# Optimization experiments

Measured on AMD Instinct MI355X. Metric: run time of the kernel, lower is better.

## Reference

```python
import jax, jax.numpy as jnp
import numpy as np

WS = 8          # window size
NUM_HEADS = 12


def setup_inputs() -> dict:
    key = jax.random.key(0)
    k1, k2, k3 = jax.random.split(key, 3)
    B, N, C = 16, 4096, 384
    x = jax.random.normal(k1, (B, N, C), dtype=jnp.float32)
    # torch Linear weights stored as [in, out] so forward is x @ W
    qkv_w = jax.random.normal(k2, (C, 3 * C), dtype=jnp.float32) * (C ** -0.5)
    proj_w = jax.random.normal(k3, (C, C), dtype=jnp.float32) * (C ** -0.5)
    proj_b = jnp.zeros((C,), dtype=jnp.float32)
    return {"x": x, "qkv_w": qkv_w, "proj_w": proj_w, "proj_b": proj_b}


def reference(x, qkv_w, proj_w, proj_b):
    B, N, C = x.shape
    H = W = int(np.sqrt(N))
    hg, wg = H // WS, W // WS
    G = hg * wg
    nh = NUM_HEADS
    hd = C // nh
    scale = hd ** -0.5

    # window partition: [B, N, C] -> [B, hg, wg, ws, ws, C]
    xw = x.reshape(B, hg, WS, wg, WS, C).transpose(0, 1, 3, 2, 4, 5)
    xw = xw.reshape(B, G, WS * WS, C)

    # qkv projection -> [3, B, G, nh, ws*ws, hd]
    qkv = (xw @ qkv_w).reshape(B, G, WS * WS, 3, nh, hd)
    qkv = qkv.transpose(3, 0, 1, 4, 2, 5)
    q, k, v = qkv[0], qkv[1], qkv[2]

    attn = jnp.einsum('bgnqd,bgnkd->bgnqk', q, k) * scale
    attn = jax.nn.softmax(attn, axis=-1)
    out = jnp.einsum('bgnqk,bgnkd->bgnqd', attn, v)

    # merge heads and reverse window partition
    out = out.transpose(0, 1, 3, 2, 4).reshape(B, hg, wg, WS, WS, C)
    out = out.transpose(0, 1, 3, 2, 4, 5).reshape(B, N, C)

    return out @ proj_w + proj_b
```

## Files before the change

kernel.cpp:

```cpp
#include <hip/hip_runtime.h>
#include <stdint.h>

typedef unsigned short ushort_t;
typedef __bf16 bf16x8 __attribute__((ext_vector_type(8)));
typedef float floatx4 __attribute__((ext_vector_type(4)));
typedef unsigned short ushort8 __attribute__((ext_vector_type(8)));

__device__ __forceinline__ ushort_t f2b(float f) {
  union { float f; unsigned u; } v; v.f = f;
  unsigned r = v.u + 0x7fffu + ((v.u >> 16) & 1u);
  return (ushort_t)(r >> 16);
}
__device__ __forceinline__ ushort_t b2u(float f) {
  union { __bf16 b; ushort_t u; } v; v.b = (__bf16)f; return v.u;
}
__device__ __forceinline__ bf16x8 cvt8(const float* p) {
  floatx4 f0 = *(const floatx4*)p;
  floatx4 f1 = *(const floatx4*)(p + 4);
  union { bf16x8 v; __bf16 e[8]; } u;
#pragma unroll
  for (int j = 0; j < 4; ++j) u.e[j] = (__bf16)f0[j];
#pragma unroll
  for (int j = 0; j < 4; ++j) u.e[4 + j] = (__bf16)f1[j];
  return u.v;
}

__device__ __forceinline__ void async16(const ushort_t* g, ushort_t* l) {
  __builtin_amdgcn_global_load_lds(
      (const __attribute__((address_space(1))) void*)g,
      (__attribute__((address_space(3))) void*)l, 16, 0, 0);
}

__global__ __launch_bounds__(256) void cvt_x(const float* __restrict__ src,
                                             ushort_t* __restrict__ dst, int n8) {
  int i = blockIdx.x * 256 + threadIdx.x;
  if (i < n8) *(bf16x8*)&dst[(size_t)i * 8] = cvt8(src + (size_t)i * 8);
}

__global__ void transpose_k(const float* __restrict__ src,
                            ushort_t* __restrict__ dst, int R, int Cc) {
  int idx = blockIdx.x * 256 + threadIdx.x;
  if (idx < R * Cc) {
    int r = idx / Cc, c = idx % Cc;
    dst[(size_t)c * R + r] = f2b(src[idx]);
  }
}

template <int C_F32>
__global__ __launch_bounds__(256) void gemm_bt(
    const ushort_t* __restrict__ A, int lda,
    const ushort_t* __restrict__ Bt,
    const float* __restrict__ bias, void* __restrict__ C_,
    int M, int N, int K) {
  __shared__ __align__(16) ushort_t As[128 * 64];
  __shared__ __align__(16) ushort_t Bs[128 * 64];
  const int t = threadIdx.x;

  const int nwg = gridDim.x;
  const int per = nwg >> 3;
  const int swz = (blockIdx.x & 7) * per + (blockIdx.x >> 3);
  const int ntn = N >> 7;
  const int m0 = (swz / ntn) << 7;
  const int n0 = (swz % ntn) << 7;

  const int w = t >> 6, lane = t & 63;
  const int wy = (w >> 1) << 6;
  const int wx = (w & 1) << 6;
  const int l15 = lane & 15;
  const int quad = lane >> 4;
  const int quad4 = quad << 2;

  floatx4 acc[4][4] = {};

  const int srow = t >> 3;
  const int sc = (((t & 7) ^ (srow & 7)) << 3);
  const ushort_t* gA = A + (size_t)(m0 + srow) * lda + sc;
  const ushort_t* gB = Bt + (size_t)(n0 + srow) * K + sc;

  for (int k0 = 0; k0 < K; k0 += 64) {
    __syncthreads();
#pragma unroll
    for (int r4 = 0; r4 < 4; ++r4) {
      async16(gA + (size_t)r4 * 32 * lda + k0, &As[r4 * 2048 + t * 8]);
      async16(gB + (size_t)r4 * 32 * K + k0, &Bs[r4 * 2048 + t * 8]);
    }
    __syncthreads();
#pragma unroll
    for (int kk = 0; kk < 2; ++kk) {
      bf16x8 af[4], bfr[4];
#pragma unroll
      for (int i = 0; i < 4; ++i) {
        int row = wy + i * 16 + l15;
        af[i] = *(const bf16x8*)&As[row * 64 + ((((kk << 2) | quad) ^ (row & 7)) << 3)];
      }
#pragma unroll
      for (int j = 0; j < 4; ++j) {
        int row = wx + j * 16 + l15;
        bfr[j] = *(const bf16x8*)&Bs[row * 64 + ((((kk << 2) | quad) ^ (row & 7)) << 3)];
      }
#pragma unroll
      for (int i = 0; i < 4; ++i)
#pragma unroll
        for (int j = 0; j < 4; ++j)
          acc[i][j] = __builtin_amdgcn_mfma_f32_16x16x32_bf16(
              af[i], bfr[j], acc[i][j], 0, 0, 0);
    }
  }

  float bv[4] = {0.f, 0.f, 0.f, 0.f};
  if (bias != nullptr) {
#pragma unroll
    for (int j = 0; j < 4; ++j) bv[j] = bias[n0 + wx + j * 16 + l15];
  }
#pragma unroll
  for (int i = 0; i < 4; ++i) {
#pragma unroll
    for (int r = 0; r < 4; ++r) {
      size_t row = (size_t)(m0 + wy + i * 16 + quad4 + r);
      if (C_F32) {
        float* cp = (float*)C_ + row * N + (n0 + wx + l15);
#pragma unroll
        for (int j = 0; j < 4; ++j) cp[j * 16] = acc[i][j][r] + bv[j];
      } else {
        ushort_t* cp = (ushort_t*)C_ + row * N + (n0 + wx + l15);
#pragma unroll
        for (int j = 0; j < 4; ++j) cp[j * 16] = f2b(acc[i][j][r] + bv[j]);
      }
    }
  }
}

__global__ __launch_bounds__(256, 2) void win_attn(
    const ushort_t* __restrict__ QKV, ushort_t* __restrict__ O, int ostride) {
  __shared__ __align__(16) ushort_t Plds[4][64 * 40];
  __shared__ __align__(16) ushort_t Vt[4][32 * 72];
  const int blk = blockIdx.x;
  const int b = blk >> 6, g = blk & 63;
  const int gy = g >> 3, gx = g & 7;
  const int t = threadIdx.x, w = t >> 6, lane = t & 63;
  const int l15 = lane & 15, quad = lane >> 4;
  const int q8 = quad << 3, quad4 = quad << 2;
  const size_t bbase = (size_t)b * 4096 + (size_t)(gy * 8) * 64 + gx * 8;
  const float scale = 0.17677669529663687f;

  bf16x8 ones;
  {
    union { bf16x8 v; __bf16 e[8]; } u;
#pragma unroll
    for (int j = 0; j < 8; ++j) u.e[j] = (__bf16)1.0f;
    ones = u.v;
  }

  for (int hi = 0; hi < 3; ++hi) {
    const int h = w * 3 + hi;
    const size_t hq = (size_t)h * 32;

    {
      size_t row = bbase + (size_t)(lane >> 3) * 64 + (lane & 7);
      const ushort_t* vp = QKV + row * 1152 + 768 + hq;
#pragma unroll
      for (int i = 0; i < 4; ++i) {
        ushort8 vv = *(const ushort8*)(vp + i * 8);
#pragma unroll
        for (int j = 0; j < 8; ++j) Vt[w][(i * 8 + j) * 72 + lane] = vv[j];
      }
    }

    bf16x8 qf[4], kf[4];
#pragma unroll
    for (int i = 0; i < 4; ++i) {
      int tok = i * 16 + l15;
      size_t row = bbase + (size_t)(tok >> 3) * 64 + (tok & 7);
      qf[i] = *(const bf16x8*)(QKV + row * 1152 + hq + q8);
      kf[i] = *(const bf16x8*)(QKV + row * 1152 + 384 + hq + q8);
    }

    floatx4 s[4][4] = {};
#pragma unroll
    for (int i = 0; i < 4; ++i)
#pragma unroll
      for (int j = 0; j < 4; ++j)
        s[i][j] = __builtin_amdgcn_mfma_f32_16x16x32_bf16(
            qf[i], kf[j], s[i][j], 0, 0, 0);

    floatx4 o[4][2] = {};
    floatx4 osum[4] = {};
#pragma unroll
    for (int ks = 0; ks < 2; ++ks) {
#pragma unroll
      for (int i = 0; i < 4; ++i) {
#pragma unroll
        for (int r = 0; r < 4; ++r) {
          float p0 = __expf(s[i][2 * ks][r] * scale);
          float p1 = __expf(s[i][2 * ks + 1][r] * scale);
          int pr = (i * 16 + quad4 + r) * 40 + l15;
          Plds[w][pr] = b2u(p0);
          Plds[w][pr + 16] = b2u(p1);
        }
      }
      bf16x8 pf[4], vf[2];
#pragma unroll
      for (int i = 0; i < 4; ++i)
        pf[i] = *(const bf16x8*)&Plds[w][(i * 16 + l15) * 40 + q8];
#pragma unroll
      for (int j = 0; j < 2; ++j)
        vf[j] = *(const bf16x8*)&Vt[w][(j * 16 + l15) * 72 + ks * 32 + q8];
#pragma unroll
      for (int i = 0; i < 4; ++i) {
#pragma unroll
        for (int j = 0; j < 2; ++j)
          o[i][j] = __builtin_amdgcn_mfma_f32_16x16x32_bf16(
              pf[i], vf[j], o[i][j], 0, 0, 0);
        osum[i] = __builtin_amdgcn_mfma_f32_16x16x32_bf16(
            pf[i], ones, osum[i], 0, 0, 0);
      }
    }

#pragma unroll
    for (int i = 0; i < 4; ++i) {
#pragma unroll
      for (int r = 0; r < 4; ++r) {
        int tok = i * 16 + quad4 + r;
        size_t row = bbase + (size_t)(tok >> 3) * 64 + (tok & 7);
        float inv = 1.0f / osum[i][r];
        ushort_t* op = O + row * (size_t)ostride + hq;
#pragma unroll
        for (int j = 0; j < 2; ++j) op[j * 16 + l15] = b2u(o[i][j][r] * inv);
      }
    }
  }
}

extern "C" void kernel_launch(void* const* d_in, const int* in_sizes, int n_in,
                              void* d_out, int out_size, void* d_ws, size_t ws_size,
                              hipStream_t stream) {
  const float* x      = (const float*)d_in[0];
  const float* qkv_w  = (const float*)d_in[1];
  const float* proj_w = (const float*)d_in[2];
  const float* proj_b = (const float*)d_in[3];
  float* out = (float*)d_out;

  const int M = 16 * 4096;
  const size_t need =
      ((size_t)M * 1152 + (size_t)M * 384 + 1152 * 384 + 384 * 384) * 2;
  if (ws_size < need) return;

  ushort_t* qkv    = (ushort_t*)d_ws;
  ushort_t* xb     = qkv + (size_t)M * 1152;
  ushort_t* qkvwT  = xb + (size_t)M * 384;
  ushort_t* projwT = qkvwT + (size_t)1152 * 384;

  cvt_x<<<(M * 384 / 8 + 255) / 256, 256, 0, stream>>>(x, xb, M * 384 / 8);
  transpose_k<<<(384 * 1152 + 255) / 256, 256, 0, stream>>>(qkv_w, qkvwT, 384, 1152);
  transpose_k<<<(384 * 384 + 255) / 256, 256, 0, stream>>>(proj_w, projwT, 384, 384);

  gemm_bt<0><<<(M / 128) * (1152 / 128), 256, 0, stream>>>(
      xb, 384, qkvwT, nullptr, qkv, M, 1152, 384);

  win_attn<<<16 * 64, 256, 0, stream>>>(qkv, qkv, 1152);

  gemm_bt<1><<<(M / 128) * (384 / 128), 256, 0, stream>>>(
      qkv, 1152, projwT, proj_b, out, M, 384, 384);
}
```

Measured before the change: 337.3 us.

## Add 8-wave triple-buffered pipelined GEMM with interleaved prefetch for both projections

Adds a new GEMM kernel with 512 threads and 256x128 tiles. It triple-buffers LDS through dynamic shared memory, so async global-to-LDS loads for tile k+2 are issued while MFMAs run on tile k. The block splits compute into four phases that interleave prefetch issue, barriers and s_setprio around MFMA groups, replacing the old load-then-compute loop with two syncthreads per k-step. The cost is one block per CU, large LDS use, and more complex vmcnt bookkeeping, with the old kernel kept as a fallback if the attribute call fails.

```diff
diff --git a/kernel.cpp b/kernel.cpp
--- a/kernel.cpp
+++ b/kernel.cpp
@@ -43,6 +43,140 @@
   if (idx < R * Cc) {
     int r = idx / Cc, c = idx % Cc;
     dst[(size_t)c * R + r] = f2b(src[idx]);
+  }
+}
+
+template <int C_F32>
+__global__ __launch_bounds__(512, 1) void gemm_p8(
+    const ushort_t* __restrict__ A, int lda,
+    const ushort_t* __restrict__ Bt,
+    const float* __restrict__ bias, void* __restrict__ C_,
+    int M, int N, int K) {
+  extern __shared__ __align__(16) ushort_t lds[];
+  ushort_t* ldsA = lds;
+  ushort_t* ldsB = lds + 3 * 16384;
+  const int t = threadIdx.x;
+
+  const int nwg = gridDim.x;
+  const int per = nwg >> 3;
+  const int swz = (blockIdx.x & 7) * per + (blockIdx.x >> 3);
+  const int ntn = N >> 7;
+  const int m0 = (swz / ntn) << 8;
+  const int n0 = (swz % ntn) << 7;
+
+  const int w = t >> 6, lane = t & 63;
+  const int wm = w >> 1, wn = w & 1;
+  const int l15 = lane & 15, quad = lane >> 4;
+  const int quad4 = quad << 2;
+
+  floatx4 acc[4][4] = {};
+
+  const int srow = t >> 3;
+  const int sc = (((t & 7) ^ (srow & 7)) << 3);
+  const int dLds = srow * 64 + (t & 7) * 8;
+  const ushort_t* gA = A + (size_t)(m0 + srow) * lda + sc;
+  const ushort_t* gB = Bt + (size_t)(n0 + srow) * K + sc;
+
+  auto stageA = [&](int buf, int c, int kofs) {
+    async16(gA + (size_t)(c * 64) * lda + kofs,
+            &ldsA[buf * 16384 + c * 4096 + dLds]);
+  };
+  auto stageB = [&](int buf, int c, int kofs) {
+    async16(gB + (size_t)(c * 64) * K + kofs,
+            &ldsB[buf * 8192 + c * 4096 + dLds]);
+  };
+  auto stage_tile = [&](int tile) {
+    const int buf = tile % 3, kofs = tile << 6;
+    stageA(buf, 0, kofs); stageA(buf, 1, kofs);
+    stageA(buf, 2, kofs); stageA(buf, 3, kofs);
+    stageB(buf, 0, kofs); stageB(buf, 1, kofs);
+  };
+
+  const int NT = K >> 6;
+  stage_tile(0);
+  stage_tile(1);
+  asm volatile("s_waitcnt vmcnt(6)" ::: "memory");
+  __builtin_amdgcn_s_barrier();
+
+  for (int kt = 0; kt < NT; ++kt) {
+    const int buf = kt % 3;
+    const ushort_t* Ab = &ldsA[buf * 16384];
+    const ushort_t* Bb = &ldsB[buf * 8192];
+    const int pt = kt + 2;
+    const bool dopf = pt < NT;
+    const int pbuf = pt % 3;
+    const int pk = pt << 6;
+
+    bf16x8 afc[2][2];
+#pragma unroll
+    for (int p = 0; p < 4; ++p) {
+      const int qi = p >> 1, qj = p & 1;
+      if (qj == 0) {
+#pragma unroll
+        for (int ii = 0; ii < 2; ++ii) {
+          const int row = wm * 64 + (qi * 2 + ii) * 16 + l15;
+#pragma unroll
+          for (int kk = 0; kk < 2; ++kk)
+            afc[ii][kk] = *(const bf16x8*)&Ab[row * 64 +
+                ((((kk << 2) | quad) ^ (row & 7)) << 3)];
+        }
+      }
+      bf16x8 bfr[2][2];
+#pragma unroll
+      for (int jj = 0; jj < 2; ++jj) {
+        const int row = wn * 64 + (qj * 2 + jj) * 16 + l15;
+#pragma unroll
+        for (int kk = 0; kk < 2; ++kk)
+          bfr[jj][kk] = *(const bf16x8*)&Bb[row * 64 +
+              ((((kk << 2) | quad) ^ (row & 7)) << 3)];
+      }
+      if (dopf) {
+        if (p == 0)      { stageA(pbuf, 0, pk); stageA(pbuf, 1, pk); }
+        else if (p == 1) { stageA(pbuf, 2, pk); stageA(pbuf, 3, pk); }
+        else if (p == 2) { stageB(pbuf, 0, pk); }
+        else             { stageB(pbuf, 1, pk); }
+      }
+      __builtin_amdgcn_s_barrier();
+      __builtin_amdgcn_s_setprio(1);
+#pragma unroll
+      for (int ii = 0; ii < 2; ++ii)
+#pragma unroll
+        for (int jj = 0; jj < 2; ++jj)
+#pragma unroll
+          for (int kk = 0; kk < 2; ++kk)
+            acc[qi * 2 + ii][qj * 2 + jj] =
+                __builtin_amdgcn_mfma_f32_16x16x32_bf16(
+                    afc[ii][kk], bfr[jj][kk], acc[qi * 2 + ii][qj * 2 + jj],
+                    0, 0, 0);
+      __builtin_amdgcn_s_setprio(0);
+      if (p == 3 && kt < NT - 1) {
+        if (dopf) asm volatile("s_waitcnt vmcnt(6)" ::: "memory");
+        else      asm volatile("s_waitcnt vmcnt(0)" ::: "memory");
+      }
+      __builtin_amdgcn_s_barrier();
+    }
+  }
+
+  float bv[4] = {0.f, 0.f, 0.f, 0.f};
+  if (bias != nullptr) {
+#pragma unroll
+    for (int j = 0; j < 4; ++j) bv[j] = bias[n0 + wn * 64 + j * 16 + l15];
+  }
+#pragma unroll
+  for (int i = 0; i < 4; ++i) {
+#pragma unroll
+    for (int r = 0; r < 4; ++r) {
+      size_t row = (size_t)(m0 + wm * 64 + i * 16 + quad4 + r);
+      if (C_F32) {
+        float* cp = (float*)C_ + row * N + (n0 + wn * 64 + l15);
+#pragma unroll
+        for (int j = 0; j < 4; ++j) cp[j * 16] = acc[i][j][r] + bv[j];
+      } else {
+        ushort_t* cp = (ushort_t*)C_ + row * N + (n0 + wn * 64 + l15);
+#pragma unroll
+        for (int j = 0; j < 4; ++j) cp[j * 16] = f2b(acc[i][j][r] + bv[j]);
+      }
+    }
   }
 }
 
@@ -55,28 +189,23 @@
   __shared__ __align__(16) ushort_t As[128 * 64];
   __shared__ __align__(16) ushort_t Bs[128 * 64];
   const int t = threadIdx.x;
-
   const int nwg = gridDim.x;
   const int per = nwg >> 3;
   const int swz = (blockIdx.x & 7) * per + (blockIdx.x >> 3);
   const int ntn = N >> 7;
   const int m0 = (swz / ntn) << 7;
   const int n0 = (swz % ntn) << 7;
-
   const int w = t >> 6, lane = t & 63;
   const int wy = (w >> 1) << 6;
   const int wx = (w & 1) << 6;
   const int l15 = lane & 15;
   const int quad = lane >> 4;
   const int quad4 = quad << 2;
-
   floatx4 acc[4][4] = {};
-
   const int srow = t >> 3;
   const int sc = (((t & 7) ^ (srow & 7)) << 3);
   const ushort_t* gA = A + (size_t)(m0 + srow) * lda + sc;
   const ushort_t* gB = Bt + (size_t)(n0 + srow) * K + sc;
-
   for (int k0 = 0; k0 < K; k0 += 64) {
     __syncthreads();
 #pragma unroll
@@ -106,7 +235,6 @@
               af[i], bfr[j], acc[i][j], 0, 0, 0);
     }
   }
-
   float bv[4] = {0.f, 0.f, 0.f, 0.f};
   if (bias != nullptr) {
 #pragma unroll
@@ -250,15 +378,36 @@
   ushort_t* qkvwT  = xb + (size_t)M * 384;
   ushort_t* projwT = qkvwT + (size_t)1152 * 384;
 
+  static bool p8init = false, p8ok = false;
+  if (!p8init) {
+    p8ok = (hipFuncSetAttribute(
+                reinterpret_cast<const void*>(gemm_p8<0>),
+                hipFuncAttributeMaxDynamicSharedMemorySize, 147456) == hipSuccess) &&
+           (hipFuncSetAttribute(
+                reinterpret_cast<const void*>(gemm_p8<1>),
+                hipFuncAttributeMaxDynamicSharedMemorySize, 147456) == hipSuccess);
+    p8init = true;
+  }
+
   cvt_x<<<(M * 384 / 8 + 255) / 256, 256, 0, stream>>>(x, xb, M * 384 / 8);
   transpose_k<<<(384 * 1152 + 255) / 256, 256, 0, stream>>>(qkv_w, qkvwT, 384, 1152);
   transpose_k<<<(384 * 384 + 255) / 256, 256, 0, stream>>>(proj_w, projwT, 384, 384);
 
-  gemm_bt<0><<<(M / 128) * (1152 / 128), 256, 0, stream>>>(
-      xb, 384, qkvwT, nullptr, qkv, M, 1152, 384);
+  if (p8ok) {
+    gemm_p8<0><<<(M / 256) * (1152 / 128), 512, 147456, stream>>>(
+        xb, 384, qkvwT, nullptr, qkv, M, 1152, 384);
+  } else {
+    gemm_bt<0><<<(M / 128) * (1152 / 128), 256, 0, stream>>>(
+        xb, 384, qkvwT, nullptr, qkv, M, 1152, 384);
+  }
 
   win_attn<<<16 * 64, 256, 0, stream>>>(qkv, qkv, 1152);
 
-  gemm_bt<1><<<(M / 128) * (384 / 128), 256, 0, stream>>>(
-      qkv, 1152, projwT, proj_b, out, M, 384, 384);
-}
+  if (p8ok) {
+    gemm_p8<1><<<(M / 256) * (384 / 128), 512, 147456, stream>>>(
+        qkv, 1152, projwT, proj_b, out, M, 384, 384);
+  } else {
+    gemm_bt<1><<<(M / 128) * (384 / 128), 256, 0, stream>>>(
+        qkv, 1152, projwT, proj_b, out, M, 384, 384);
+  }
+}
```

Measured after the change: 364.8 us. +8.1%, slower.

## Use 32x32 MFMA with register-resident softmax in window attention

Applied to the files above, without the earlier changes.

Rewrites the window-attention kernel to compute S^T = K·Q^T with 32x32x16 MFMAs so each lane holds a key column, then computes exp and row sums in registers with a cross-half shuffle. The probability matrix is converted to bf16 with packed converts and rearranged via permlane32 swaps into the A-operand layout, removing the LDS round-trip for P and the extra ones-MFMA used for row sums. Normalisation is applied before the PV product instead of after. This adds inline asm tied to gfx950 instructions and a more intricate register layout, and it still omits max subtraction.

```diff
diff --git a/kernel.cpp b/kernel.cpp
--- a/kernel.cpp
+++ b/kernel.cpp
@@ -4,6 +4,7 @@
 typedef unsigned short ushort_t;
 typedef __bf16 bf16x8 __attribute__((ext_vector_type(8)));
 typedef float floatx4 __attribute__((ext_vector_type(4)));
+typedef float floatx16 __attribute__((ext_vector_type(16)));
 typedef unsigned short ushort8 __attribute__((ext_vector_type(8)));
 
 __device__ __forceinline__ ushort_t f2b(float f) {
@@ -23,6 +24,15 @@
 #pragma unroll
   for (int j = 0; j < 4; ++j) u.e[4 + j] = (__bf16)f1[j];
   return u.v;
+}
+
+__device__ __forceinline__ unsigned cvtpk(float a, float b) {
+  unsigned r;
+  asm("v_cvt_pk_bf16_f32 %0, %1, %2" : "=v"(r) : "v"(a), "v"(b));
+  return r;
+}
+__device__ __forceinline__ void plswap(unsigned& x, unsigned& y) {
+  asm("v_permlane32_swap_b32 %0, %1" : "+v"(x), "+v"(y));
 }
 
 __device__ __forceinline__ void async16(const ushort_t* g, ushort_t* l) {
@@ -55,28 +65,23 @@
   __shared__ __align__(16) ushort_t As[128 * 64];
   __shared__ __align__(16) ushort_t Bs[128 * 64];
   const int t = threadIdx.x;
-
   const int nwg = gridDim.x;
   const int per = nwg >> 3;
   const int swz = (blockIdx.x & 7) * per + (blockIdx.x >> 3);
   const int ntn = N >> 7;
   const int m0 = (swz / ntn) << 7;
   const int n0 = (swz % ntn) << 7;
-
   const int w = t >> 6, lane = t & 63;
   const int wy = (w >> 1) << 6;
   const int wx = (w & 1) << 6;
   const int l15 = lane & 15;
   const int quad = lane >> 4;
   const int quad4 = quad << 2;
-
   floatx4 acc[4][4] = {};
-
   const int srow = t >> 3;
   const int sc = (((t & 7) ^ (srow & 7)) << 3);
   const ushort_t* gA = A + (size_t)(m0 + srow) * lda + sc;
   const ushort_t* gB = Bt + (size_t)(n0 + srow) * K + sc;
-
   for (int k0 = 0; k0 < K; k0 += 64) {
     __syncthreads();
 #pragma unroll
@@ -106,7 +111,6 @@
               af[i], bfr[j], acc[i][j], 0, 0, 0);
     }
   }
-
   float bv[4] = {0.f, 0.f, 0.f, 0.f};
   if (bias != nullptr) {
 #pragma unroll
@@ -132,24 +136,14 @@
 
 __global__ __launch_bounds__(256, 2) void win_attn(
     const ushort_t* __restrict__ QKV, ushort_t* __restrict__ O, int ostride) {
-  __shared__ __align__(16) ushort_t Plds[4][64 * 40];
   __shared__ __align__(16) ushort_t Vt[4][32 * 72];
   const int blk = blockIdx.x;
   const int b = blk >> 6, g = blk & 63;
   const int gy = g >> 3, gx = g & 7;
   const int t = threadIdx.x, w = t >> 6, lane = t & 63;
-  const int l15 = lane & 15, quad = lane >> 4;
-  const int q8 = quad << 3, quad4 = quad << 2;
+  const int l31 = lane & 31, bh = lane >> 5;
   const size_t bbase = (size_t)b * 4096 + (size_t)(gy * 8) * 64 + gx * 8;
   const float scale = 0.17677669529663687f;
-
-  bf16x8 ones;
-  {
-    union { bf16x8 v; __bf16 e[8]; } u;
-#pragma unroll
-    for (int j = 0; j < 8; ++j) u.e[j] = (__bf16)1.0f;
-    ones = u.v;
-  }
 
   for (int hi = 0; hi < 3; ++hi) {
     const int h = w * 3 + hi;
@@ -166,68 +160,76 @@
       }
     }
 
-    bf16x8 qf[4], kf[4];
-#pragma unroll
-    for (int i = 0; i < 4; ++i) {
-      int tok = i * 16 + l15;
+    bf16x8 qf[2][2];
+#pragma unroll
+    for (int qt = 0; qt < 2; ++qt) {
+      int tok = qt * 32 + l31;
       size_t row = bbase + (size_t)(tok >> 3) * 64 + (tok & 7);
-      qf[i] = *(const bf16x8*)(QKV + row * 1152 + hq + q8);
-      kf[i] = *(const bf16x8*)(QKV + row * 1152 + 384 + hq + q8);
-    }
-
-    floatx4 s[4][4] = {};
-#pragma unroll
-    for (int i = 0; i < 4; ++i)
-#pragma unroll
-      for (int j = 0; j < 4; ++j)
-        s[i][j] = __builtin_amdgcn_mfma_f32_16x16x32_bf16(
-            qf[i], kf[j], s[i][j], 0, 0, 0);
-
-    floatx4 o[4][2] = {};
-    floatx4 osum[4] = {};
-#pragma unroll
-    for (int ks = 0; ks < 2; ++ks) {
-#pragma unroll
-      for (int i = 0; i < 4; ++i) {
-#pragma unroll
-        for (int r = 0; r < 4; ++r) {
-          float p0 = __expf(s[i][2 * ks][r] * scale);
-          float p1 = __expf(s[i][2 * ks + 1][r] * scale);
-          int pr = (i * 16 + quad4 + r) * 40 + l15;
-          Plds[w][pr] = b2u(p0);
-          Plds[w][pr + 16] = b2u(p1);
+#pragma unroll
+      for (int dc = 0; dc < 2; ++dc)
+        qf[qt][dc] = *(const bf16x8*)(QKV + row * 1152 + hq + dc * 16 + bh * 8);
+    }
+
+    floatx16 st[2][2] = {};
+#pragma unroll
+    for (int kt = 0; kt < 2; ++kt) {
+      bf16x8 kf[2];
+      int tok = kt * 32 + l31;
+      size_t row = bbase + (size_t)(tok >> 3) * 64 + (tok & 7);
+#pragma unroll
+      for (int dc = 0; dc < 2; ++dc)
+        kf[dc] = *(const bf16x8*)(QKV + row * 1152 + 384 + hq + dc * 16 + bh * 8);
+#pragma unroll
+      for (int qt = 0; qt < 2; ++qt)
+#pragma unroll
+        for (int dc = 0; dc < 2; ++dc)
+          st[kt][qt] = __builtin_amdgcn_mfma_f32_32x32x16_bf16(
+              kf[dc], qf[qt][dc], st[kt][qt], 0, 0, 0);
+    }
+
+    float rs[2] = {0.f, 0.f};
+#pragma unroll
+    for (int kt = 0; kt < 2; ++kt)
+#pragma unroll
+      for (int qt = 0; qt < 2; ++qt)
+#pragma unroll
+        for (int r = 0; r < 16; ++r) {
+          float e = __expf(st[kt][qt][r] * scale);
+          st[kt][qt][r] = e;
+          rs[qt] += e;
         }
-      }
-      bf16x8 pf[4], vf[2];
-#pragma unroll
-      for (int i = 0; i < 4; ++i)
-        pf[i] = *(const bf16x8*)&Plds[w][(i * 16 + l15) * 40 + q8];
-#pragma unroll
-      for (int j = 0; j < 2; ++j)
-        vf[j] = *(const bf16x8*)&Vt[w][(j * 16 + l15) * 72 + ks * 32 + q8];
-#pragma unroll
-      for (int i = 0; i < 4; ++i) {
-#pragma unroll
-        for (int j = 0; j < 2; ++j)
-          o[i][j] = __builtin_amdgcn_mfma_f32_16x16x32_bf16(
-              pf[i], vf[j], o[i][j], 0, 0, 0);
-        osum[i] = __builtin_amdgcn_mfma_f32_16x16x32_bf16(
-            pf[i], ones, osum[i], 0, 0, 0);
-      }
-    }
-
-#pragma unroll
-    for (int i = 0; i < 4; ++i) {
-#pragma unroll
-      for (int r = 0; r < 4; ++r) {
-        int tok = i * 16 + quad4 + r;
+#pragma unroll
+    for (int qt = 0; qt < 2; ++qt) rs[qt] += __shfl_xor(rs[qt], 32);
+    float inv[2] = {1.0f / rs[0], 1.0f / rs[1]};
+
+    floatx16 o[2] = {};
+#pragma unroll
+    for (int s = 0; s < 4; ++s) {
+      const int kt = s >> 1, r1x = (s & 1) << 1;
+      bf16x8 vf = *(const bf16x8*)&Vt[w][l31 * 72 + s * 16 + bh * 8];
+#pragma unroll
+      for (int qt = 0; qt < 2; ++qt) {
+        float iv = inv[qt];
+        unsigned x0 = cvtpk(st[kt][qt][4 * r1x + 0] * iv, st[kt][qt][4 * r1x + 1] * iv);
+        unsigned x1 = cvtpk(st[kt][qt][4 * r1x + 2] * iv, st[kt][qt][4 * r1x + 3] * iv);
+        unsigned y0 = cvtpk(st[kt][qt][4 * r1x + 4] * iv, st[kt][qt][4 * r1x + 5] * iv);
+        unsigned y1 = cvtpk(st[kt][qt][4 * r1x + 6] * iv, st[kt][qt][4 * r1x + 7] * iv);
+        plswap(x0, y0);
+        plswap(x1, y1);
+        union { unsigned d[4]; bf16x8 v; } pa;
+        pa.d[0] = x0; pa.d[1] = x1; pa.d[2] = y0; pa.d[3] = y1;
+        o[qt] = __builtin_amdgcn_mfma_f32_32x32x16_bf16(pa.v, vf, o[qt], 0, 0, 0);
+      }
+    }
+
+#pragma unroll
+    for (int qt = 0; qt < 2; ++qt)
+#pragma unroll
+      for (int r = 0; r < 16; ++r) {
+        int tok = qt * 32 + (r & 3) + 8 * (r >> 2) + 4 * bh;
         size_t row = bbase + (size_t)(tok >> 3) * 64 + (tok & 7);
-        float inv = 1.0f / osum[i][r];
-        ushort_t* op = O + row * (size_t)ostride + hq;
-#pragma unroll
-        for (int j = 0; j < 2; ++j) op[j * 16 + l15] = b2u(o[i][j][r] * inv);
-      }
-    }
+        O[row * (size_t)ostride + hq + l31] = b2u(o[qt][r]);
+      }
   }
 }
 
```

Measured after the change: 342.1 us. About the same (+1.4%).
